# Kernel tuning notes

Measured on AMD Instinct MI355X. Metric: run time of the kernel, lower is better.

## Reference

```python
import jax, jax.numpy as jnp
import numpy as np

N_CODES = 4096
D = 256


def setup_inputs() -> dict:
    key = jax.random.key(0)
    k_v, k_w = jax.random.split(key)
    v = jax.random.normal(k_v, (8, 2048, D), dtype=jnp.float32)
    # Embedding init ~ N(0,1), then softmax over dim=1, then row 0 set to 1/d (empty feature)
    w = jax.random.normal(k_w, (N_CODES, D), dtype=jnp.float32)
    w = jax.nn.softmax(w, axis=1)
    w = w.at[0].set(1.0 / D)
    return {"v": v, "vectors": w}


def reference(v, vectors):
    n, d = vectors.shape
    cb = vectors[1:]  # exclude the fixed empty feature at index 0
    # ||v - c||^2 = ||v||^2 - 2 v.c + ||c||^2  (avoids [..., n, d] intermediate)
    v2 = jnp.sum(v * v, axis=-1, keepdims=True)              # [..., 1]
    c2 = jnp.sum(cb * cb, axis=-1)                           # [n-1]
    diff = v2 - 2.0 * jnp.einsum('...d,nd->...n', v, cb) + c2  # [..., n-1]
    idx = jnp.argmin(diff, axis=-1) + 1                      # [...]
    # empty-feature mask: any component differs from 1/d
    mask = jnp.any(v != (1.0 / d), axis=-1)
    idx = jnp.where(mask, idx, 0)
    out = vectors[idx]                                       # gather == onehot @ vectors
    loss = jnp.mean(jnp.square(out - jax.lax.stop_gradient(v)))
    used = jnp.array(0, dtype=jnp.int32)  # eval mode: usage pool is empty
    return out, idx, loss, used
```

## Files before the change

kernel.cpp:

```cpp
#include <hip/hip_runtime.h>
#include <hip/hip_fp16.h>
#include <math.h>
#include <stdint.h>


#define M_TOTAL 16384
#define NCODES  4096
#define D_DIM   256

#define OUT_OFF_IDX  (M_TOTAL * D_DIM)
#define OUT_OFF_LOSS (OUT_OFF_IDX + M_TOTAL)

#define NPART 16
#define VPLANE (M_TOTAL * D_DIM)

typedef _Float16 half8 __attribute__((ext_vector_type(8)));
typedef _Float16 half4v __attribute__((ext_vector_type(4)));
typedef float    float16v __attribute__((ext_vector_type(16)));

__global__ __launch_bounds__(64) void prep_v_kernel(
    const float* __restrict__ X, _Float16* __restrict__ hi, _Float16* __restrict__ lo,
    float* __restrict__ sq)
{
  __shared__ float T[64 * 66];
  const int l = threadIdx.x;
  const int r0 = blockIdx.x * 64;
  float rj[8];
  float s0 = 0.0f, s1 = 0.0f;
#pragma unroll
  for (int kt = 0; kt < 4; ++kt) {
    __syncthreads();
#pragma unroll
    for (int s = 0; s < 16; ++s) {
      const int row = s * 4 + (l >> 4), c4 = l & 15;
      const size_t go = (size_t)(r0 + row) * D_DIM + kt * 64 + c4 * 4;
      float4 v = *(const float4*)(X + go);
      float xs[4] = {v.x, v.y, v.z, v.w};
      union { half4v h; _Float16 e[4]; } uh, ul;
#pragma unroll
      for (int j = 0; j < 4; ++j) {
        float sc = xs[j] * 1024.0f;
        _Float16 h = (_Float16)sc;
        uh.e[j] = h;
        ul.e[j] = (_Float16)(sc - (float)h);
      }
      *(half4v*)(hi + go) = uh.h;
      *(half4v*)(lo + go) = ul.h;
      *(float4*)&T[row * 66 + c4 * 4] = v;
    }
    __syncthreads();
#pragma unroll
    for (int c4 = 0; c4 < 16; ++c4) {
      float4 v = *(const float4*)&T[l * 66 + c4 * 4];
      float e[4] = {v.x, v.y, v.z, v.w};
#pragma unroll
      for (int t = 0; t < 4; ++t) {
        const int k = kt * 64 + c4 * 4 + t;
        const int j = k & 7;
        float sqv = __fmul_rn(e[t], e[t]);
        if ((k & 127) < 8) rj[j] = sqv;
        else rj[j] = __fadd_rn(rj[j], sqv);
      }
    }
    if (kt == 1) s0 = __fadd_rn(__fadd_rn(__fadd_rn(rj[0], rj[1]), __fadd_rn(rj[2], rj[3])),
                                __fadd_rn(__fadd_rn(rj[4], rj[5]), __fadd_rn(rj[6], rj[7])));
    if (kt == 3) s1 = __fadd_rn(__fadd_rn(__fadd_rn(rj[0], rj[1]), __fadd_rn(rj[2], rj[3])),
                                __fadd_rn(__fadd_rn(rj[4], rj[5]), __fadd_rn(rj[6], rj[7])));
  }
  sq[r0 + l] = __fadd_rn(s0, s1);
}

__global__ __launch_bounds__(64) void prep_w_kernel(
    const float* __restrict__ W, _Float16* __restrict__ Bp, float* __restrict__ c2)
{
  __shared__ float T[64 * 66];
  const int l = threadIdx.x;
  const int r0 = blockIdx.x * 64;
  const int panel = (r0 >> 5) + (l >> 5);
  const int nin = l & 31;
  float rj[8];
  float s0 = 0.0f, s1 = 0.0f;
#pragma unroll
  for (int kt = 0; kt < 4; ++kt) {
    __syncthreads();
#pragma unroll
    for (int s = 0; s < 16; ++s) {
      const int row = s * 4 + (l >> 4), c4 = l & 15;
      *(float4*)&T[row * 66 + c4 * 4] =
          *(const float4*)(W + (size_t)(r0 + row) * D_DIM + kt * 64 + c4 * 4);
    }
    __syncthreads();
    union { half8 v; _Float16 e[8]; } uh, ul;
#pragma unroll
    for (int c4 = 0; c4 < 16; ++c4) {
      float4 v = *(const float4*)&T[l * 66 + c4 * 4];
      float e[4] = {v.x, v.y, v.z, v.w};
#pragma unroll
      for (int t = 0; t < 4; ++t) {
        const int k = kt * 64 + c4 * 4 + t;
        float sc = e[t] * 1024.0f;
        _Float16 h = (_Float16)sc;
        uh.e[(c4 & 1) * 4 + t] = h;
        ul.e[(c4 & 1) * 4 + t] = (_Float16)(sc - (float)h);
        const int j = k & 7;
        float sqv = __fmul_rn(e[t], e[t]);
        if ((k & 127) < 8) rj[j] = sqv;
        else rj[j] = __fadd_rn(rj[j], sqv);
      }
      if (c4 & 1) {
        const int g = kt * 8 + (c4 >> 1);
        const int kstep = g >> 1, lhi = g & 1;
        _Float16* dst = Bp + ((size_t)panel * 16 + kstep) * 2048 + lhi * 256 + nin * 8;
        *(half8*)dst = uh.v;
        *(half8*)(dst + 1024) = ul.v;
      }
    }
    if (kt == 1) s0 = __fadd_rn(__fadd_rn(__fadd_rn(rj[0], rj[1]), __fadd_rn(rj[2], rj[3])),
                                __fadd_rn(__fadd_rn(rj[4], rj[5]), __fadd_rn(rj[6], rj[7])));
    if (kt == 3) s1 = __fadd_rn(__fadd_rn(__fadd_rn(rj[0], rj[1]), __fadd_rn(rj[2], rj[3])),
                                __fadd_rn(__fadd_rn(rj[4], rj[5]), __fadd_rn(rj[6], rj[7])));
  }
  c2[r0 + l] = __fadd_rn(s0, s1);
}

__global__ __launch_bounds__(256, 2) void vq_mfma_kernel(
    const _Float16* __restrict__ Vhi, const _Float16* __restrict__ Vlo,
    const _Float16* __restrict__ Bp,
    const float* __restrict__ v2, const float* __restrict__ c2,
    uint64_t* __restrict__ pk)
{
  __shared__ __align__(16) _Float16 lds[16384];

  const int tid  = threadIdx.x;
  const int lane = tid & 63;
  const int wave = tid >> 6;
  const int wr = wave >> 1, wc = wave & 1;
  const int l31 = lane & 31, lhi = lane >> 5;
  const int m0 = blockIdx.x * 128;
  const int n0 = blockIdx.y * 256;
  const int panelBase = (n0 >> 5) + wc * 4;

  int src[4], dst8[4];
#pragma unroll
  for (int u = 0; u < 4; ++u) {
    const int q = tid + 256 * u, m = q >> 3, kb = q & 7;
    src[u]  = (m0 + m) * D_DIM + kb * 8;
    dst8[u] = m * 64 + (kb ^ (m & 7)) * 8;
  }

  float16v acc[2][4];
#pragma unroll
  for (int mb = 0; mb < 2; ++mb)
#pragma unroll
    for (int nb = 0; nb < 4; ++nb) acc[mb][nb] = (float16v)0.0f;

  half8 sh[4], sl[4];
#pragma unroll
  for (int u = 0; u < 4; ++u) {
    sh[u] = *(const half8*)(Vhi + src[u]);
    sl[u] = *(const half8*)(Vlo + src[u]);
  }

  for (int kt = 0; kt < 4; ++kt) {
    if (kt) __syncthreads();
#pragma unroll
    for (int u = 0; u < 4; ++u) {
      *(half8*)(lds + dst8[u])        = sh[u];
      *(half8*)(lds + 8192 + dst8[u]) = sl[u];
    }
    __syncthreads();
    if (kt < 3) {
#pragma unroll
      for (int u = 0; u < 4; ++u) {
        sh[u] = *(const half8*)(Vhi + src[u] + (kt + 1) * 64);
        sl[u] = *(const half8*)(Vlo + src[u] + (kt + 1) * 64);
      }
    }
#pragma unroll
    for (int ks = 0; ks < 4; ++ks) {
      const int kstep = kt * 4 + ks;
      half8 ah[2], al[2];
#pragma unroll
      for (int mb = 0; mb < 2; ++mb) {
        const int m = wr * 64 + mb * 32 + l31;
        const int c = (ks * 2 + lhi) ^ (m & 7);
        ah[mb] = *(const half8*)(lds + m * 64 + c * 8);
        al[mb] = *(const half8*)(lds + 8192 + m * 64 + c * 8);
      }
      half8 bh[4], bl[4];
#pragma unroll
      for (int nb = 0; nb < 4; ++nb) {
        const _Float16* bp = Bp + ((size_t)(panelBase + nb) * 16 + kstep) * 2048 + lane * 8;
        bh[nb] = *(const half8*)bp;
        bl[nb] = *(const half8*)(bp + 1024);
      }
#pragma unroll
      for (int nb = 0; nb < 4; ++nb)
#pragma unroll
        for (int mb = 0; mb < 2; ++mb)
          acc[mb][nb] = __builtin_amdgcn_mfma_f32_32x32x16_f16(ah[mb], bh[nb], acc[mb][nb], 0, 0, 0);
#pragma unroll
      for (int nb = 0; nb < 4; ++nb)
#pragma unroll
        for (int mb = 0; mb < 2; ++mb)
          acc[mb][nb] = __builtin_amdgcn_mfma_f32_32x32x16_f16(ah[mb], bl[nb], acc[mb][nb], 0, 0, 0);
#pragma unroll
      for (int nb = 0; nb < 4; ++nb)
#pragma unroll
        for (int mb = 0; mb < 2; ++mb)
          acc[mb][nb] = __builtin_amdgcn_mfma_f32_32x32x16_f16(al[mb], bh[nb], acc[mb][nb], 0, 0, 0);
    }
  }

  float c2r[4];
#pragma unroll
  for (int nb = 0; nb < 4; ++nb) c2r[nb] = c2[n0 + wc * 128 + nb * 32 + l31];

  __syncthreads();
  uint64_t* red = (uint64_t*)lds;

#pragma unroll
  for (int mb = 0; mb < 2; ++mb) {
#pragma unroll
    for (int r = 0; r < 16; ++r) {
      const int mloc = wr * 64 + mb * 32 + (r & 3) + 8 * (r >> 2) + 4 * lhi;
      const float v2m = v2[m0 + mloc];
      uint64_t b = ~0ULL;
#pragma unroll
      for (int nb = 0; nb < 4; ++nb) {
        const int n = n0 + wc * 128 + nb * 32 + l31;
        float dot = acc[mb][nb][r] * 0x1p-20f;
        float dd  = __fadd_rn(__fsub_rn(v2m, 2.0f * dot), c2r[nb]);
        if (n == 0) dd = INFINITY;
        uint64_t p = ((uint64_t)__float_as_uint(dd) << 32) | (uint32_t)n;
        if (p < b) b = p;
      }
#pragma unroll
      for (int off = 16; off; off >>= 1) {
        uint64_t o = __shfl_xor((unsigned long long)b, off);
        if (o < b) b = o;
      }
      if (l31 == 0) red[mloc * 2 + wc] = b;
    }
  }
  __syncthreads();
  if (tid < 128) {
    uint64_t a0 = red[tid * 2], a1 = red[tid * 2 + 1];
    pk[blockIdx.y * M_TOTAL + m0 + tid] = a0 < a1 ? a0 : a1;
  }
}

__global__ __launch_bounds__(256) void gather_kernel(
    const float* __restrict__ V, const float* __restrict__ W,
    const uint64_t* __restrict__ pk,
    float* __restrict__ out, float* __restrict__ outIdx,
    float* __restrict__ lossPartial)
{
  const int q = blockIdx.x * 4 + (threadIdx.x >> 6);
  const int l = threadIdx.x & 63;
  uint64_t b = (l < NPART) ? pk[(size_t)l * M_TOTAL + q] : ~0ULL;
#pragma unroll
  for (int off = 32; off; off >>= 1) {
    uint64_t o = __shfl_xor((unsigned long long)b, off);
    if (o < b) b = o;
  }
  float4 vv = *(const float4*)(V + (size_t)q * D_DIM + l * 4);
  const float inv = 0.00390625f;
  bool ne = (vv.x != inv) | (vv.y != inv) | (vv.z != inv) | (vv.w != inv);
  const int idx = __ballot(ne) ? (int)(uint32_t)b : 0;
  float4 o4 = *(const float4*)(W + (size_t)idx * D_DIM + l * 4);
  *(float4*)(out + (size_t)q * D_DIM + l * 4) = o4;
  if (l == 0) outIdx[q] = (float)idx;
  float dx = o4.x - vv.x, dy = o4.y - vv.y, dz = o4.z - vv.z, dw = o4.w - vv.w;
  float s = dx * dx + dy * dy + dz * dz + dw * dw;
#pragma unroll
  for (int off = 32; off; off >>= 1) s += __shfl_xor(s, off);
  if (l == 0) lossPartial[q] = s;
}

__global__ __launch_bounds__(256) void finalize_kernel(
    const float* __restrict__ lossPartial, float* __restrict__ out)
{
  const int t = threadIdx.x;
  __shared__ float red[256];
  float s = 0.0f;
  for (int i = t; i < M_TOTAL; i += 256) s += lossPartial[i];
  red[t] = s;
  __syncthreads();
  for (int st = 128; st > 0; st >>= 1) {
    if (t < st) red[t] += red[t + st];
    __syncthreads();
  }
  if (t == 0) {
    out[0] = (float)((double)red[0] / (double)(M_TOTAL * D_DIM));
    out[1] = 0.0f;
  }
}

extern "C" void kernel_launch(void* const* d_in, const int* in_sizes, int n_in,
                              void* d_out, int out_size, void* d_ws, size_t ws_size,
                              hipStream_t stream) {
  const float* V = (const float*)d_in[0];
  const float* W = (const float*)d_in[1];
  float* out = (float*)d_out;

  _Float16* Vhi = (_Float16*)d_out;
  _Float16* Vlo = Vhi + VPLANE;

  char* ws = (char*)d_ws;
  _Float16* Bp  = (_Float16*)(ws);
  float*    c2  = (float*)(ws + 8388608);
  float*    v2  = (float*)(ws + 8388608 + 16384);
  uint64_t* pk  = (uint64_t*)(ws + 8388608 + 16384 + 65536);
  float* lossPartial = (float*)(ws + 8388608 + 16384 + 65536 + 2097152);

  prep_w_kernel<<<NCODES / 64, 64, 0, stream>>>(W, Bp, c2);
  prep_v_kernel<<<M_TOTAL / 64, 64, 0, stream>>>(V, Vhi, Vlo, v2);
  vq_mfma_kernel<<<dim3(M_TOTAL / 128, NCODES / 256), 256, 0, stream>>>(Vhi, Vlo, Bp, v2, c2, pk);
  gather_kernel<<<M_TOTAL / 4, 256, 0, stream>>>(V, W, pk, out, out + OUT_OFF_IDX, lossPartial);
  finalize_kernel<<<1, 256, 0, stream>>>(lossPartial, out + OUT_OFF_LOSS);
}
```

Before: 236.6 us.

## Enlarge MFMA tile to 256 rows, double-buffer codebook loads, remap block order

The distance GEMM block tile grows from 128 to 256 rows of v, so each wave holds a 4x4 accumulator set, and the K loop is split into eight 32-wide LDS stages. Codebook fragments are now loaded one k-step ahead into a double-buffered register set. A 1D grid with a swizzled block-to-panel mapping is meant to improve L2 reuse of codebook panels. The argmin reduction moves from cross-lane shuffles to an LDS-staged reduction. The larger accumulator raises register pressure, so occupancy drops to one block per SIMD group, and the extra syncs per row block add overhead.

```diff
diff --git a/kernel.cpp b/kernel.cpp
--- a/kernel.cpp
+++ b/kernel.cpp
@@ -123,34 +123,39 @@
   c2[r0 + l] = __fadd_rn(s0, s1);
 }
 
-__global__ __launch_bounds__(256, 2) void vq_mfma_kernel(
+__global__ __launch_bounds__(256, 1) void vq_mfma_kernel(
     const _Float16* __restrict__ Vhi, const _Float16* __restrict__ Vlo,
     const _Float16* __restrict__ Bp,
     const float* __restrict__ v2, const float* __restrict__ c2,
     uint64_t* __restrict__ pk)
 {
-  __shared__ __align__(16) _Float16 lds[16384];
+  __shared__ __align__(16) _Float16 smem[16384];
+  __shared__ uint64_t red2[512];
 
   const int tid  = threadIdx.x;
   const int lane = tid & 63;
   const int wave = tid >> 6;
   const int wr = wave >> 1, wc = wave & 1;
   const int l31 = lane & 31, lhi = lane >> 5;
-  const int m0 = blockIdx.x * 128;
-  const int n0 = blockIdx.y * 256;
-  const int panelBase = (n0 >> 5) + wc * 4;
-
-  int src[4], dst8[4];
+
+  const int bid = blockIdx.x;
+  const int panel = (bid & 7) * 2 + ((bid >> 3) & 1);
+  const int mblk  = bid >> 4;
+  const int m0 = mblk * 256;
+  const int n0 = panel * 256;
+  const int p32 = (n0 >> 5) + wc * 4;
+
+  int src[4], dst[4];
 #pragma unroll
   for (int u = 0; u < 4; ++u) {
-    const int q = tid + 256 * u, m = q >> 3, kb = q & 7;
-    src[u]  = (m0 + m) * D_DIM + kb * 8;
-    dst8[u] = m * 64 + (kb ^ (m & 7)) * 8;
-  }
-
-  float16v acc[2][4];
-#pragma unroll
-  for (int mb = 0; mb < 2; ++mb)
+    const int g = tid + 256 * u, m = g >> 2, kb = g & 3;
+    src[u] = (m0 + m) * D_DIM + kb * 8;
+    dst[u] = m * 32 + (kb ^ (m & 3)) * 8;
+  }
+
+  float16v acc[4][4];
+#pragma unroll
+  for (int mb = 0; mb < 4; ++mb)
 #pragma unroll
     for (int nb = 0; nb < 4; ++nb) acc[mb][nb] = (float16v)0.0f;
 
@@ -161,54 +166,65 @@
     sl[u] = *(const half8*)(Vlo + src[u]);
   }
 
-  for (int kt = 0; kt < 4; ++kt) {
+  half8 bh[2][4], bl[2][4];
+#pragma unroll
+  for (int nb = 0; nb < 4; ++nb) {
+    const _Float16* bp = Bp + ((size_t)(p32 + nb) * 16 + 0) * 2048 + lane * 8;
+    bh[0][nb] = *(const half8*)bp;
+    bl[0][nb] = *(const half8*)(bp + 1024);
+  }
+
+#pragma unroll
+  for (int kt = 0; kt < 8; ++kt) {
     if (kt) __syncthreads();
 #pragma unroll
     for (int u = 0; u < 4; ++u) {
-      *(half8*)(lds + dst8[u])        = sh[u];
-      *(half8*)(lds + 8192 + dst8[u]) = sl[u];
-    }
-    __syncthreads();
-    if (kt < 3) {
+      *(half8*)(smem + dst[u])        = sh[u];
+      *(half8*)(smem + 8192 + dst[u]) = sl[u];
+    }
+    __syncthreads();
+    if (kt < 7) {
 #pragma unroll
       for (int u = 0; u < 4; ++u) {
-        sh[u] = *(const half8*)(Vhi + src[u] + (kt + 1) * 64);
-        sl[u] = *(const half8*)(Vlo + src[u] + (kt + 1) * 64);
-      }
-    }
-#pragma unroll
-    for (int ks = 0; ks < 4; ++ks) {
-      const int kstep = kt * 4 + ks;
-      half8 ah[2], al[2];
-#pragma unroll
-      for (int mb = 0; mb < 2; ++mb) {
-        const int m = wr * 64 + mb * 32 + l31;
-        const int c = (ks * 2 + lhi) ^ (m & 7);
-        ah[mb] = *(const half8*)(lds + m * 64 + c * 8);
-        al[mb] = *(const half8*)(lds + 8192 + m * 64 + c * 8);
-      }
-      half8 bh[4], bl[4];
-#pragma unroll
-      for (int nb = 0; nb < 4; ++nb) {
-        const _Float16* bp = Bp + ((size_t)(panelBase + nb) * 16 + kstep) * 2048 + lane * 8;
-        bh[nb] = *(const half8*)bp;
-        bl[nb] = *(const half8*)(bp + 1024);
+        sh[u] = *(const half8*)(Vhi + src[u] + (kt + 1) * 32);
+        sl[u] = *(const half8*)(Vlo + src[u] + (kt + 1) * 32);
+      }
+    }
+#pragma unroll
+    for (int ks = 0; ks < 2; ++ks) {
+      const int kstep = kt * 2 + ks;
+      const int cur = kstep & 1, nxt = cur ^ 1;
+      if (kstep < 15) {
+#pragma unroll
+        for (int nb = 0; nb < 4; ++nb) {
+          const _Float16* bp = Bp + ((size_t)(p32 + nb) * 16 + kstep + 1) * 2048 + lane * 8;
+          bh[nxt][nb] = *(const half8*)bp;
+          bl[nxt][nb] = *(const half8*)(bp + 1024);
+        }
+      }
+      half8 ah[4], al[4];
+#pragma unroll
+      for (int mb = 0; mb < 4; ++mb) {
+        const int m = wr * 128 + mb * 32 + l31;
+        const int c = (ks * 2 + lhi) ^ (m & 3);
+        ah[mb] = *(const half8*)(smem + m * 32 + c * 8);
+        al[mb] = *(const half8*)(smem + 8192 + m * 32 + c * 8);
       }
 #pragma unroll
       for (int nb = 0; nb < 4; ++nb)
 #pragma unroll
-        for (int mb = 0; mb < 2; ++mb)
-          acc[mb][nb] = __builtin_amdgcn_mfma_f32_32x32x16_f16(ah[mb], bh[nb], acc[mb][nb], 0, 0, 0);
+        for (int mb = 0; mb < 4; ++mb)
+          acc[mb][nb] = __builtin_amdgcn_mfma_f32_32x32x16_f16(ah[mb], bh[cur][nb], acc[mb][nb], 0, 0, 0);
 #pragma unroll
       for (int nb = 0; nb < 4; ++nb)
 #pragma unroll
-        for (int mb = 0; mb < 2; ++mb)
-          acc[mb][nb] = __builtin_amdgcn_mfma_f32_32x32x16_f16(ah[mb], bl[nb], acc[mb][nb], 0, 0, 0);
+        for (int mb = 0; mb < 4; ++mb)
+          acc[mb][nb] = __builtin_amdgcn_mfma_f32_32x32x16_f16(ah[mb], bl[cur][nb], acc[mb][nb], 0, 0, 0);
 #pragma unroll
       for (int nb = 0; nb < 4; ++nb)
 #pragma unroll
-        for (int mb = 0; mb < 2; ++mb)
-          acc[mb][nb] = __builtin_amdgcn_mfma_f32_32x32x16_f16(al[mb], bh[nb], acc[mb][nb], 0, 0, 0);
+        for (int mb = 0; mb < 4; ++mb)
+          acc[mb][nb] = __builtin_amdgcn_mfma_f32_32x32x16_f16(al[mb], bh[cur][nb], acc[mb][nb], 0, 0, 0);
     }
   }
 
@@ -217,14 +233,14 @@
   for (int nb = 0; nb < 4; ++nb) c2r[nb] = c2[n0 + wc * 128 + nb * 32 + l31];
 
   __syncthreads();
-  uint64_t* red = (uint64_t*)lds;
-
-#pragma unroll
-  for (int mb = 0; mb < 2; ++mb) {
+  uint64_t* wbuf = (uint64_t*)smem + wave * 1024;
+
+#pragma unroll
+  for (int mb = 0; mb < 4; ++mb) {
 #pragma unroll
     for (int r = 0; r < 16; ++r) {
-      const int mloc = wr * 64 + mb * 32 + (r & 3) + 8 * (r >> 2) + 4 * lhi;
-      const float v2m = v2[m0 + mloc];
+      const int mrow = wr * 128 + mb * 32 + (r & 3) + 8 * (r >> 2) + 4 * lhi;
+      const float v2m = v2[m0 + mrow];
       uint64_t b = ~0ULL;
 #pragma unroll
       for (int nb = 0; nb < 4; ++nb) {
@@ -235,19 +251,28 @@
         uint64_t p = ((uint64_t)__float_as_uint(dd) << 32) | (uint32_t)n;
         if (p < b) b = p;
       }
-#pragma unroll
-      for (int off = 16; off; off >>= 1) {
-        uint64_t o = __shfl_xor((unsigned long long)b, off);
-        if (o < b) b = o;
-      }
-      if (l31 == 0) red[mloc * 2 + wc] = b;
-    }
-  }
-  __syncthreads();
-  if (tid < 128) {
-    uint64_t a0 = red[tid * 2], a1 = red[tid * 2 + 1];
-    pk[blockIdx.y * M_TOTAL + m0 + tid] = a0 < a1 ? a0 : a1;
-  }
+      wbuf[r * 64 + lhi * 32 + l31] = b;
+    }
+    __syncthreads();
+    {
+      const int f = lane >> 1, hf = lane & 1;
+      const uint64_t* rp = wbuf + f * 32 + hf * 16;
+      uint64_t m = rp[0];
+#pragma unroll
+      for (int i = 1; i < 16; ++i) { uint64_t v = rp[i]; if (v < m) m = v; }
+      uint64_t o = __shfl_xor((unsigned long long)m, 1);
+      if (o < m) m = o;
+      if (hf == 0) {
+        const int r_ = f >> 1, lh2 = f & 1;
+        const int mrow = wr * 128 + mb * 32 + (r_ & 3) + 8 * (r_ >> 2) + 4 * lh2;
+        red2[mrow * 2 + wc] = m;
+      }
+    }
+    __syncthreads();
+  }
+
+  uint64_t a0 = red2[tid * 2], a1 = red2[tid * 2 + 1];
+  pk[(size_t)panel * M_TOTAL + m0 + tid] = a0 < a1 ? a0 : a1;
 }
 
 __global__ __launch_bounds__(256) void gather_kernel(
@@ -316,7 +341,7 @@
 
   prep_w_kernel<<<NCODES / 64, 64, 0, stream>>>(W, Bp, c2);
   prep_v_kernel<<<M_TOTAL / 64, 64, 0, stream>>>(V, Vhi, Vlo, v2);
-  vq_mfma_kernel<<<dim3(M_TOTAL / 128, NCODES / 256), 256, 0, stream>>>(Vhi, Vlo, Bp, v2, c2, pk);
+  vq_mfma_kernel<<<1024, 256, 0, stream>>>(Vhi, Vlo, Bp, v2, c2, pk);
   gather_kernel<<<M_TOTAL / 4, 256, 0, stream>>>(V, W, pk, out, out + OUT_OFF_IDX, lossPartial);
   finalize_kernel<<<1, 256, 0, stream>>>(lossPartial, out + OUT_OFF_LOSS);
 }
```

New measurement: 223.4 us. 1.06x faster.
